# Kernel tuning notes

Hardware: AMD Instinct MI355X
Metric: run time of the kernel (lower is better)

The kernel has to match this reference:

```python
import jax, jax.numpy as jnp
import numpy as np
import math

D_MODEL = 512
D_HEAD = 64
N_HEADS = D_MODEL // D_HEAD  # 8
COND = 768
K = 7        # neighborhood kernel size
EPS = 1e-6


def _rope_freqs():
    # RoPE(dim=d_head//2, n_heads): freqs geometric in [pi, 10*pi), shape [n_heads, d_head//4]
    dim = D_HEAD // 2
    n = N_HEADS * dim // 2
    freqs = jnp.exp(jnp.linspace(math.log(math.pi), math.log(10.0 * math.pi), n + 1)[:-1])
    return freqs.reshape(dim // 2, N_HEADS).T  # [nh, d_head//4]


def _rms_norm(x, scale, eps):
    mean_sq = jnp.mean(x * x, axis=-1, keepdims=True)
    return x * (scale * jax.lax.rsqrt(mean_sq + eps))


def _apply_rotary(x, theta):
    # rotate first 2*d dims of head dim, leave the rest untouched
    d = theta.shape[-1]
    x1, x2, rest = x[..., :d], x[..., d:2 * d], x[..., 2 * d:]
    cos, sin = jnp.cos(theta), jnp.sin(theta)
    return jnp.concatenate([x1 * cos - x2 * sin, x2 * cos + x1 * sin, rest], axis=-1)


def _nb_idx(L, k):
    # NATTEN border handling: window shifts (clamps) so every query sees exactly k keys
    i = np.arange(L)
    start = np.clip(i - k // 2, 0, L - k)
    return jnp.asarray(start[:, None] + np.arange(k)[None, :])  # [L, k]


def setup_inputs() -> dict:
    key = jax.random.key(0)
    ks = jax.random.split(key, 7)
    N, H, W = 2, 32, 32
    x = jax.random.normal(ks[0], (N, H, W, D_MODEL), jnp.float32)
    pos = jax.random.uniform(ks[1], (N, H, W, 1), jnp.float32, -1.0, 1.0)
    cond = jax.random.normal(ks[2], (N, COND), jnp.float32)
    w_cond = jax.random.normal(ks[3], (D_MODEL, COND), jnp.float32) * 0.02
    w_qkv = jax.random.normal(ks[4], (3 * D_MODEL, D_MODEL), jnp.float32) * 0.02
    scale = jnp.full((N_HEADS,), 10.0, jnp.float32)
    w_out = jax.random.normal(ks[5], (D_MODEL, D_MODEL), jnp.float32) * 0.02
    return {"x": x, "pos": pos, "cond": cond, "w_cond": w_cond,
            "w_qkv": w_qkv, "scale": scale, "w_out": w_out}


def reference(x, pos, cond, w_cond, w_qkv, scale, w_out):
    N, H, W, C = x.shape
    skip = x
    # AdaRMSNorm: rms_norm(x, linear(cond) + 1)
    norm_scale = cond @ w_cond.T + 1.0                  # [N, C]
    xn = _rms_norm(x, norm_scale[:, None, None, :], EPS)
    # qkv projection -> [3, N, nh, H, W, e]
    qkv = (xn @ w_qkv.T).reshape(N, H, W, 3, N_HEADS, D_HEAD)
    qkv = qkv.transpose(3, 0, 4, 1, 2, 5)
    q, k, v = qkv[0], qkv[1], qkv[2]                    # [N, nh, H, W, e]
    # cosine-sim scaling
    sq = jnp.sqrt(scale)[:, None, None, None]           # [nh,1,1,1]
    q = q * (sq * jax.lax.rsqrt(jnp.sum(q * q, -1, keepdims=True) + 1e-6))
    k = k * (sq * jax.lax.rsqrt(jnp.sum(k * k, -1, keepdims=True) + 1e-6))
    # RoPE
    theta = pos[..., None, :] * _rope_freqs()           # [N,H,W,nh,e/4]
    theta = jnp.moveaxis(theta, -2, -4)                 # [N,nh,H,W,e/4]
    q = _apply_rotary(q, theta)
    k = _apply_rotary(k, theta)
    # 2D neighborhood attention (NATTEN, dilation 1)
    ih, iw = _nb_idx(H, K), _nb_idx(W, K)
    Knb = k[:, :, ih][:, :, :, :, iw]                   # [N,nh,H,K,W,K,e]
    Vnb = v[:, :, ih][:, :, :, :, iw]
    qk = jnp.einsum('ncije,nciajbe->ncijab', q, Knb)    # [N,nh,H,W,K,K]
    a = jax.nn.softmax(qk.reshape(N, N_HEADS, H, W, K * K), axis=-1)
    a = a.reshape(N, N_HEADS, H, W, K, K)
    o = jnp.einsum('ncijab,nciajbe->ncije', a, Vnb)     # [N,nh,H,W,e]
    o = o.transpose(0, 2, 3, 1, 4).reshape(N, H, W, C)
    return o @ w_out.T + skip
```

## Files before the change

### kernel.cpp

```cpp
#include <hip/hip_runtime.h>

typedef unsigned short u16;
typedef unsigned int u32;
typedef __bf16 bf16x8 __attribute__((ext_vector_type(8)));
typedef float f32x4 __attribute__((ext_vector_type(4)));

__device__ __forceinline__ float bf2f(u16 v) {
    union { u32 u; float f; } c; c.u = ((u32)v) << 16; return c.f;
}
__device__ __forceinline__ u16 f2bf(float f) {
    union { float f; u32 u; } c; c.f = f;
    u32 u = c.u + 0x7fffu + ((c.u >> 16) & 1u);
    return (u16)(u >> 16);
}

__global__ __launch_bounds__(256) void cond_prepw_kernel(
    const float* __restrict__ cond, const float* __restrict__ w_cond, float* __restrict__ ns,
    const float* __restrict__ w_qkv, const float* __restrict__ w_out,
    u16* __restrict__ wqkvb, u16* __restrict__ woutb)
{
    int b = blockIdx.x;
    if (b < 256) {
        int lane = threadIdx.x & 63;
        int wid = b * 4 + (threadIdx.x >> 6);
        int n = wid >> 9, c = wid & 511;
        const float* cp = cond + n * 768;
        const float* wp = w_cond + (size_t)c * 768;
        float s = 0.f;
        #pragma unroll
        for (int j = 0; j < 12; j++)
            s += cp[lane + j * 64] * wp[lane + j * 64];
        #pragma unroll
        for (int d = 1; d < 64; d <<= 1) s += __shfl_xor(s, d);
        if (lane == 0) ns[wid] = s + 1.f;
    } else {
        const float* src; u16* dst; size_t i4;
        if (b < 1024) { src = w_qkv; dst = wqkvb; i4 = (size_t)(b - 256)  * 1024 + threadIdx.x * 4; }
        else          { src = w_out; dst = woutb; i4 = (size_t)(b - 1024) * 1024 + threadIdx.x * 4; }
        float4 v = *(const float4*)(src + i4);
        ushort4 o; o.x = f2bf(v.x); o.y = f2bf(v.y); o.z = f2bf(v.z); o.w = f2bf(v.w);
        *(ushort4*)(dst + i4) = o;
    }
}

__global__ __launch_bounds__(256) void rms_kernel(
    const float* __restrict__ x, const float* __restrict__ ns, u16* __restrict__ xn)
{
    int b = blockIdx.x;
    int w = threadIdx.x >> 6, lane = threadIdx.x & 63;
    int p = b * 4 + w;
    int n = p >> 10;
    const float* xp = x + (size_t)p * 512;
    const float* nsp = ns + n * 512;
    float4 v0 = *(const float4*)(xp + lane * 4);
    float4 v1 = *(const float4*)(xp + 256 + lane * 4);
    float ss = v0.x * v0.x + v0.y * v0.y + v0.z * v0.z + v0.w * v0.w
             + v1.x * v1.x + v1.y * v1.y + v1.z * v1.z + v1.w * v1.w;
    #pragma unroll
    for (int d = 1; d < 64; d <<= 1) ss += __shfl_xor(ss, d);
    float inv = rsqrtf(ss * (1.f / 512.f) + 1e-6f);
    float4 n0 = *(const float4*)(nsp + lane * 4);
    float4 n1 = *(const float4*)(nsp + 256 + lane * 4);
    ushort4 o0, o1;
    o0.x = f2bf(v0.x * n0.x * inv); o0.y = f2bf(v0.y * n0.y * inv);
    o0.z = f2bf(v0.z * n0.z * inv); o0.w = f2bf(v0.w * n0.w * inv);
    o1.x = f2bf(v1.x * n1.x * inv); o1.y = f2bf(v1.y * n1.y * inv);
    o1.z = f2bf(v1.z * n1.z * inv); o1.w = f2bf(v1.w * n1.w * inv);
    *(ushort4*)(xn + (size_t)p * 512 + lane * 4) = o0;
    *(ushort4*)(xn + (size_t)p * 512 + 256 + lane * 4) = o1;
}

__global__ __launch_bounds__(256) void gemm_qkv(
    const u16* __restrict__ A, const u16* __restrict__ B,
    const float* __restrict__ pos, const float* __restrict__ scale,
    u16* __restrict__ qp, u16* __restrict__ kp, u16* __restrict__ vp)
{
    __shared__ __align__(16) u16 As[4][64][40];
    __shared__ __align__(16) u16 Bs[4][64][40];
    int tid = threadIdx.x;
    int lane = tid & 63;
    int w = tid >> 6;
    int wm = w >> 1, wn = w & 1;
    int bm = blockIdx.x * 64, bn = blockIdx.y * 64;
    int qk = blockIdx.y >> 3, h = blockIdx.y & 7;
    int lrow = tid >> 2, lc8 = (tid & 3) * 8;

    f32x4 zero = {0.f, 0.f, 0.f, 0.f};
    f32x4 acc[2][2];
    acc[0][0] = zero; acc[0][1] = zero; acc[1][0] = zero; acc[1][1] = zero;

    const u16* Ap = A + (size_t)(bm + lrow) * 512 + lc8;
    const u16* Bp = B + (size_t)(bn + lrow) * 512 + lc8;
    int m = lane & 15, quad = lane >> 4, kq = quad * 8;

    for (int k0 = 0; k0 < 512; k0 += 128) {
        #pragma unroll
        for (int s = 0; s < 4; s++) {
            *(uint4*)&As[s][lrow][lc8] = *(const uint4*)(Ap + k0 + s * 32);
            *(uint4*)&Bs[s][lrow][lc8] = *(const uint4*)(Bp + k0 + s * 32);
        }
        __syncthreads();
        #pragma unroll
        for (int kk = 0; kk < 4; kk++) {
            bf16x8 a0 = *(const bf16x8*)&As[kk][wm * 32 + m][kq];
            bf16x8 a1 = *(const bf16x8*)&As[kk][wm * 32 + 16 + m][kq];
            bf16x8 b0 = *(const bf16x8*)&Bs[kk][wn * 32 + m][kq];
            bf16x8 b1 = *(const bf16x8*)&Bs[kk][wn * 32 + 16 + m][kq];
            acc[0][0] = __builtin_amdgcn_mfma_f32_16x16x32_bf16(a0, b0, acc[0][0], 0, 0, 0);
            acc[0][1] = __builtin_amdgcn_mfma_f32_16x16x32_bf16(a0, b1, acc[0][1], 0, 0, 0);
            acc[1][0] = __builtin_amdgcn_mfma_f32_16x16x32_bf16(a1, b0, acc[1][0], 0, 0, 0);
            acc[1][1] = __builtin_amdgcn_mfma_f32_16x16x32_bf16(a1, b1, acc[1][1], 0, 0, 0);
        }
        __syncthreads();
    }

    float invn[2][4];
    if (qk < 2) {
        float* red = (float*)As;
        #pragma unroll
        for (int ri = 0; ri < 2; ri++)
        #pragma unroll
        for (int reg = 0; reg < 4; reg++) {
            float pa = acc[ri][0][reg] * acc[ri][0][reg]
                     + acc[ri][1][reg] * acc[ri][1][reg];
            #pragma unroll
            for (int d = 1; d < 16; d <<= 1) pa += __shfl_xor(pa, d);
            if (m == 0) red[(wm * 32 + ri * 16 + quad * 4 + reg) * 2 + wn] = pa;
        }
        __syncthreads();
        float sq = sqrtf(scale[h]);
        #pragma unroll
        for (int ri = 0; ri < 2; ri++)
        #pragma unroll
        for (int reg = 0; reg < 4; reg++) {
            int rl = wm * 32 + ri * 16 + quad * 4 + reg;
            invn[ri][reg] = sq * rsqrtf(red[rl * 2] + red[rl * 2 + 1] + 1e-6f);
        }
    }
    u16* plane = (qk == 0) ? qp : (qk == 1) ? kp : vp;
    float fr = 3.14159265358979323846f * expf((float)(m * 8 + h) * (2.302585092994046f / 128.f));
    #pragma unroll
    for (int ri = 0; ri < 2; ri++)
    #pragma unroll
    for (int reg = 0; reg < 4; reg++) {
        int rl = wm * 32 + ri * 16 + quad * 4 + reg;
        int p = bm + rl;
        size_t basep = ((size_t)((p >> 10) * 8 + h) * 1024 + (p & 1023)) * 64;
        float v0 = acc[ri][0][reg], v1 = acc[ri][1][reg];
        if (qk < 2) {
            float ivn = invn[ri][reg];
            v0 *= ivn; v1 *= ivn;
            if (wn == 0) {
                float th = pos[p] * fr;
                float cs = cosf(th), sn = sinf(th);
                float o0 = v0 * cs - v1 * sn;
                float o1 = v1 * cs + v0 * sn;
                v0 = o0; v1 = o1;
            }
        }
        plane[basep + wn * 32 + m]      = f2bf(v0);
        plane[basep + wn * 32 + 16 + m] = f2bf(v1);
    }
}

__global__ __launch_bounds__(256) void gemm_out(
    const u16* __restrict__ A, const u16* __restrict__ B,
    float* __restrict__ C, const float* __restrict__ skip, int N, int K)
{
    __shared__ __align__(16) u16 As[4][64][40];
    __shared__ __align__(16) u16 Bs[4][64][40];
    int tid = threadIdx.x;
    int lane = tid & 63;
    int w = tid >> 6;
    int wm = w >> 1, wn = w & 1;
    int bm = blockIdx.x * 64, bn = blockIdx.y * 64;
    int lrow = tid >> 2, lc8 = (tid & 3) * 8;

    f32x4 zero = {0.f, 0.f, 0.f, 0.f};
    f32x4 acc[2][2];
    acc[0][0] = zero; acc[0][1] = zero; acc[1][0] = zero; acc[1][1] = zero;

    const u16* Ap = A + (size_t)(bm + lrow) * K + lc8;
    const u16* Bp = B + (size_t)(bn + lrow) * K + lc8;
    int r = lane & 15, kq = (lane >> 4) * 8;

    for (int k0 = 0; k0 < K; k0 += 128) {
        #pragma unroll
        for (int s = 0; s < 4; s++) {
            *(uint4*)&As[s][lrow][lc8] = *(const uint4*)(Ap + k0 + s * 32);
            *(uint4*)&Bs[s][lrow][lc8] = *(const uint4*)(Bp + k0 + s * 32);
        }
        __syncthreads();
        #pragma unroll
        for (int kk = 0; kk < 4; kk++) {
            bf16x8 a0 = *(const bf16x8*)&As[kk][wm * 32 + r][kq];
            bf16x8 a1 = *(const bf16x8*)&As[kk][wm * 32 + 16 + r][kq];
            bf16x8 b0 = *(const bf16x8*)&Bs[kk][wn * 32 + r][kq];
            bf16x8 b1 = *(const bf16x8*)&Bs[kk][wn * 32 + 16 + r][kq];
            acc[0][0] = __builtin_amdgcn_mfma_f32_16x16x32_bf16(a0, b0, acc[0][0], 0, 0, 0);
            acc[0][1] = __builtin_amdgcn_mfma_f32_16x16x32_bf16(a0, b1, acc[0][1], 0, 0, 0);
            acc[1][0] = __builtin_amdgcn_mfma_f32_16x16x32_bf16(a1, b0, acc[1][0], 0, 0, 0);
            acc[1][1] = __builtin_amdgcn_mfma_f32_16x16x32_bf16(a1, b1, acc[1][1], 0, 0, 0);
        }
        __syncthreads();
    }

    #pragma unroll
    for (int ri = 0; ri < 2; ri++)
    #pragma unroll
    for (int ci = 0; ci < 2; ci++) {
        int col = bn + wn * 32 + ci * 16 + (lane & 15);
        int row0 = bm + wm * 32 + ri * 16 + (lane >> 4) * 4;
        #pragma unroll
        for (int reg = 0; reg < 4; reg++) {
            size_t idx = (size_t)(row0 + reg) * N + col;
            C[idx] = acc[ri][ci][reg] + skip[idx];
        }
    }
}

__global__ __launch_bounds__(512) void attn_mfma(
    const u16* __restrict__ qp, const u16* __restrict__ kp, const u16* __restrict__ vp,
    u16* __restrict__ ob)
{
    __shared__ __align__(16) u16 Kb[208 * 72];
    __shared__ __align__(16) u16 Sb[64 * 232];

    int tid = threadIdx.x, lane = tid & 63, w = tid >> 6;
    int bx = blockIdx.x;
    int n = bx >> 7, h = (bx >> 4) & 7, t = bx & 15;
    int ti = (t >> 2) * 8, tj = (t & 3) * 8;
    int r0 = min(max(ti - 3, 0), 18), c0 = min(max(tj - 3, 0), 18);
    const u16* qpl = qp + ((size_t)(n * 8 + h) << 16);
    const u16* kpl = kp + ((size_t)(n * 8 + h) << 16);
    const u16* vpl = vp + ((size_t)(n * 8 + h) << 16);

    for (int g = tid; g < 1568; g += 512) {
        int nb = g >> 3, k8 = (g & 7) << 3;
        int ar = nb / 14, ac = nb - ar * 14;
        *(uint4*)&Kb[nb * 72 + k8] =
            *(const uint4*)&kpl[(size_t)((r0 + ar) * 32 + c0 + ac) * 64 + k8];
    }
    __syncthreads();

    int m = lane & 15, quad = lane >> 4;
    int rg = w & 3, half = w >> 2;
    {
        int r = rg * 16 + m;
        int tok = (ti + (r >> 3)) * 32 + (tj + (r & 7));
        bf16x8 qf0 = *(const bf16x8*)&qpl[(size_t)tok * 64 + quad * 8];
        bf16x8 qf1 = *(const bf16x8*)&qpl[(size_t)tok * 64 + 32 + quad * 8];
        _Float16* sp = (_Float16*)Sb;
        int ntb = half * 7;
        int ntn = 7 - half;
        for (int i = 0; i < ntn; i++) {
            int nt = ntb + i;
            f32x4 acc = {0.f, 0.f, 0.f, 0.f};
            bf16x8 b0 = *(const bf16x8*)&Kb[(nt * 16 + m) * 72 + quad * 8];
            bf16x8 b1 = *(const bf16x8*)&Kb[(nt * 16 + m) * 72 + 32 + quad * 8];
            __builtin_amdgcn_s_setprio(1);
            acc = __builtin_amdgcn_mfma_f32_16x16x32_bf16(qf0, b0, acc, 0, 0, 0);
            acc = __builtin_amdgcn_mfma_f32_16x16x32_bf16(qf1, b1, acc, 0, 0, 0);
            __builtin_amdgcn_s_setprio(0);
            #pragma unroll
            for (int reg = 0; reg < 4; reg++)
                sp[(rg * 16 + quad * 4 + reg) * 232 + nt * 16 + m] = (_Float16)acc[reg];
        }
    }
    __syncthreads();

    for (int g = tid; g < 1568; g += 512) {
        int nb = g >> 3, k8 = (g & 7) << 3;
        int ar = nb / 14, ac = nb - ar * 14;
        uint4 v4 = *(const uint4*)&vpl[(size_t)((r0 + ar) * 32 + c0 + ac) * 64 + k8];
        u32 uu[4] = {v4.x, v4.y, v4.z, v4.w};
        #pragma unroll
        for (int e = 0; e < 4; e++) {
            Kb[(k8 + 2 * e) * 234 + nb]     = (u16)(uu[e] & 0xffff);
            Kb[(k8 + 2 * e + 1) * 234 + nb] = (u16)(uu[e] >> 16);
        }
    }
    for (int g = tid; g < 1792; g += 512) {
        int d = g / 28, nb = 196 + (g - d * 28);
        Kb[d * 234 + nb] = 0;
    }

    {
        int l16 = lane & 15, g4 = lane >> 4;
        #pragma unroll
        for (int it = 0; it < 2; it++) {
            int rr = w * 8 + it * 4 + g4;
            int i2 = ti + (rr >> 3), j2 = tj + (rr & 7);
            int alo = min(max(i2 - 3, 0), 25) - r0;
            int blo = min(max(j2 - 3, 0), 25) - c0;
            const _Float16* sp = (const _Float16*)&Sb[rr * 232];
            float vals[14];
            float mx = -1e30f;
            #pragma unroll
            for (int c = 0; c < 14; c++) {
                int col = l16 + c * 16;
                float v = -1e30f;
                if (col < 196) {
                    int ar = col / 14, ac = col - ar * 14;
                    if (ar >= alo && ar < alo + 7 && ac >= blo && ac < blo + 7)
                        v = (float)sp[col];
                }
                vals[c] = v; mx = fmaxf(mx, v);
            }
            #pragma unroll
            for (int d = 1; d < 16; d <<= 1) mx = fmaxf(mx, __shfl_xor(mx, d));
            float s = 0.f;
            #pragma unroll
            for (int c = 0; c < 14; c++) {
                float e = exp2f((vals[c] - mx) * 1.44269504f);
                vals[c] = e; s += e;
            }
            #pragma unroll
            for (int d = 1; d < 16; d <<= 1) s += __shfl_xor(s, d);
            float rs = __frcp_rn(s);
            u16* pp = &Sb[rr * 232];
            #pragma unroll
            for (int c = 0; c < 14; c++)
                pp[l16 + c * 16] = f2bf(vals[c] * rs);
        }
    }
    __syncthreads();

    f32x4 oacc[2];
    {
        f32x4 z = {0.f, 0.f, 0.f, 0.f};
        oacc[0] = z; oacc[1] = z;
    }
    #pragma unroll
    for (int ks = 0; ks < 7; ks++) {
        bf16x8 pa = *(const bf16x8*)&Sb[(rg * 16 + m) * 232 + ks * 32 + quad * 8];
        __builtin_amdgcn_s_setprio(1);
        #pragma unroll
        for (int j = 0; j < 2; j++) {
            int nt = half * 2 + j;
            int ad = (nt * 16 + m) * 234 + ks * 32 + quad * 8;
            union { u32 u[4]; bf16x8 v; } vb;
            vb.u[0] = *(const u32*)&Kb[ad];
            vb.u[1] = *(const u32*)&Kb[ad + 2];
            vb.u[2] = *(const u32*)&Kb[ad + 4];
            vb.u[3] = *(const u32*)&Kb[ad + 6];
            oacc[j] = __builtin_amdgcn_mfma_f32_16x16x32_bf16(pa, vb.v, oacc[j], 0, 0, 0);
        }
        __builtin_amdgcn_s_setprio(0);
    }
    #pragma unroll
    for (int j = 0; j < 2; j++) {
        int nt = half * 2 + j;
        #pragma unroll
        for (int reg = 0; reg < 4; reg++) {
            int rr = rg * 16 + quad * 4 + reg;
            int tok = (ti + (rr >> 3)) * 32 + (tj + (rr & 7));
            ob[(size_t)(n * 1024 + tok) * 512 + h * 64 + nt * 16 + m] = f2bf(oacc[j][reg]);
        }
    }
}

extern "C" void kernel_launch(void* const* d_in, const int* in_sizes, int n_in,
                              void* d_out, int out_size, void* d_ws, size_t ws_size,
                              hipStream_t stream)
{
    const float *x = nullptr, *pos = nullptr, *cond = nullptr, *w_cond = nullptr,
                *w_qkv = nullptr, *scale = nullptr, *w_out = nullptr;
    for (int i = 0; i < n_in; i++) {
        switch (in_sizes[i]) {
            case 1048576: x      = (const float*)d_in[i]; break;
            case 2048:    pos    = (const float*)d_in[i]; break;
            case 1536:    cond   = (const float*)d_in[i]; break;
            case 393216:  w_cond = (const float*)d_in[i]; break;
            case 786432:  w_qkv  = (const float*)d_in[i]; break;
            case 8:       scale  = (const float*)d_in[i]; break;
            case 262144:  w_out  = (const float*)d_in[i]; break;
            default: break;
        }
    }
    float* out = (float*)d_out;

    char* ws = (char*)d_ws;
    float* ns    = (float*)ws;
    u16*   wqkvb = (u16*)(ws + 12288);
    u16*   woutb = (u16*)(ws + 12288 + 1572864);
    u16*   xn    = (u16*)(ws + 12288 + 2097152);
    u16*   qp    = (u16*)(ws + 12288 + 4194304);
    u16*   kp    = (u16*)(ws + 12288 + 6291456);
    u16*   vp    = (u16*)(ws + 12288 + 8388608);
    u16*   ob    = (u16*)(ws + 12288 + 10485760);

    cond_prepw_kernel<<<1280, 256, 0, stream>>>(cond, w_cond, ns, w_qkv, w_out, wqkvb, woutb);
    rms_kernel<<<512, 256, 0, stream>>>(x, ns, xn);
    gemm_qkv<<<dim3(32, 24), 256, 0, stream>>>(xn, wqkvb, pos, scale, qp, kp, vp);
    attn_mfma<<<256, 512, 0, stream>>>(qp, kp, vp, ob);
    gemm_out<<<dim3(32, 8), 256, 0, stream>>>(ob, woutb, out, x, 512, 512);
}
```

Measured before the change: 105.2 us.

## Fuse all five stages into one cooperative persistent kernel with grid syncs

Replaces the five separate kernel launches (cond/weight prep, RMS norm, QKV GEMM, neighborhood attention, output GEMM) with one cooperative kernel of 256 blocks by 512 threads that runs each stage in turn, separated by grid-wide syncs. The goal is to remove per-launch overhead and the gaps between kernels. In exchange, every stage is fixed to 256 blocks of 512 threads, so some stages run at lower parallelism (the QKV GEMM loops three tiles per block), and each grid sync has its own cost. If the cooperative launch fails, it falls back to the old multi-kernel path.

```diff
diff --git a/kernel.cpp b/kernel.cpp
--- a/kernel.cpp
+++ b/kernel.cpp
@@ -1,4 +1,7 @@
 #include <hip/hip_runtime.h>
+#include <hip/hip_cooperative_groups.h>
+
+namespace cg = cooperative_groups;
 
 typedef unsigned short u16;
 typedef unsigned int u32;
@@ -13,6 +16,328 @@
     u32 u = c.u + 0x7fffu + ((c.u >> 16) & 1u);
     return (u16)(u >> 16);
 }
+
+__global__ __launch_bounds__(512) void fused_all(
+    const float* __restrict__ cond, const float* __restrict__ w_cond,
+    const float* __restrict__ w_qkv, const float* __restrict__ w_out,
+    const float* __restrict__ x, const float* __restrict__ pos,
+    const float* __restrict__ scale,
+    float* __restrict__ ns, u16* __restrict__ wqkvb, u16* __restrict__ woutb,
+    u16* __restrict__ xn, u16* __restrict__ qp, u16* __restrict__ kp,
+    u16* __restrict__ vp, u16* __restrict__ ob, float* __restrict__ out)
+{
+    __shared__ __align__(16) u16 SM[29824];
+    cg::grid_group gg = cg::this_grid();
+
+    int tid = threadIdx.x, lane = tid & 63, w = tid >> 6;
+    int bid = blockIdx.x;
+    int m = lane & 15, quad = lane >> 4, kq = quad * 8;
+
+    if (w < 4) {
+        int wid = bid * 4 + w;
+        int n = wid >> 9, c = wid & 511;
+        const float* cp = cond + n * 768;
+        const float* wp = w_cond + (size_t)c * 768;
+        float s = 0.f;
+        #pragma unroll
+        for (int j = 0; j < 12; j++)
+            s += cp[lane + j * 64] * wp[lane + j * 64];
+        #pragma unroll
+        for (int d = 1; d < 64; d <<= 1) s += __shfl_xor(s, d);
+        if (lane == 0) ns[wid] = s + 1.f;
+    } else {
+        int gt = (bid * 4 + (w - 4)) * 64 + lane;
+        #pragma unroll
+        for (int i = 0; i < 4; i++) {
+            int task = gt + i * 65536;
+            const float* src; u16* dst; int idx;
+            if (task < 196608) { src = w_qkv; dst = wqkvb; idx = task; }
+            else               { src = w_out; dst = woutb; idx = task - 196608; }
+            float4 v = *(const float4*)(src + (size_t)idx * 4);
+            ushort4 o; o.x = f2bf(v.x); o.y = f2bf(v.y); o.z = f2bf(v.z); o.w = f2bf(v.w);
+            *(ushort4*)(dst + (size_t)idx * 4) = o;
+        }
+    }
+    gg.sync();
+
+    {
+        int p = bid * 8 + w;
+        int n = p >> 10;
+        const float* xp = x + (size_t)p * 512;
+        const float* nsp = ns + n * 512;
+        float4 v0 = *(const float4*)(xp + lane * 4);
+        float4 v1 = *(const float4*)(xp + 256 + lane * 4);
+        float ss = v0.x * v0.x + v0.y * v0.y + v0.z * v0.z + v0.w * v0.w
+                 + v1.x * v1.x + v1.y * v1.y + v1.z * v1.z + v1.w * v1.w;
+        #pragma unroll
+        for (int d = 1; d < 64; d <<= 1) ss += __shfl_xor(ss, d);
+        float inv = rsqrtf(ss * (1.f / 512.f) + 1e-6f);
+        float4 n0 = *(const float4*)(nsp + lane * 4);
+        float4 n1 = *(const float4*)(nsp + 256 + lane * 4);
+        ushort4 o0, o1;
+        o0.x = f2bf(v0.x * n0.x * inv); o0.y = f2bf(v0.y * n0.y * inv);
+        o0.z = f2bf(v0.z * n0.z * inv); o0.w = f2bf(v0.w * n0.w * inv);
+        o1.x = f2bf(v1.x * n1.x * inv); o1.y = f2bf(v1.y * n1.y * inv);
+        o1.z = f2bf(v1.z * n1.z * inv); o1.w = f2bf(v1.w * n1.w * inv);
+        *(ushort4*)(xn + (size_t)p * 512 + lane * 4) = o0;
+        *(ushort4*)(xn + (size_t)p * 512 + 256 + lane * 4) = o1;
+    }
+    gg.sync();
+
+    {
+        u16 (*As)[64][40] = (u16 (*)[64][40])SM;
+        u16 (*Bs)[64][40] = (u16 (*)[64][40])(SM + 10240);
+        int wm = w >> 1, wn = w & 1;
+        int lrow = tid >> 3, lc16 = (tid & 7) * 16;
+        int sA = lc16 >> 5, off = lc16 & 31;
+        int rlbase = wm * 16 + quad * 4;
+
+        for (int it = 0; it < 3; it++) {
+            int t = bid + it * 256;
+            int bm = (t & 31) * 64;
+            int by = t >> 5;
+            int bn = by * 64;
+            int qk = by >> 3, h = by & 7;
+            const u16* Ap = xn + (size_t)(bm + lrow) * 512 + lc16;
+            const u16* Bp = wqkvb + (size_t)(bn + lrow) * 512 + lc16;
+            f32x4 acc0 = {0.f, 0.f, 0.f, 0.f};
+            f32x4 acc1 = {0.f, 0.f, 0.f, 0.f};
+            __syncthreads();
+            for (int k0 = 0; k0 < 512; k0 += 128) {
+                *(uint4*)&As[sA][lrow][off]     = *(const uint4*)(Ap + k0);
+                *(uint4*)&As[sA][lrow][off + 8] = *(const uint4*)(Ap + k0 + 8);
+                *(uint4*)&Bs[sA][lrow][off]     = *(const uint4*)(Bp + k0);
+                *(uint4*)&Bs[sA][lrow][off + 8] = *(const uint4*)(Bp + k0 + 8);
+                __syncthreads();
+                #pragma unroll
+                for (int kk = 0; kk < 4; kk++) {
+                    bf16x8 a  = *(const bf16x8*)&As[kk][wm * 16 + m][kq];
+                    bf16x8 b0 = *(const bf16x8*)&Bs[kk][wn * 32 + m][kq];
+                    bf16x8 b1 = *(const bf16x8*)&Bs[kk][wn * 32 + 16 + m][kq];
+                    acc0 = __builtin_amdgcn_mfma_f32_16x16x32_bf16(a, b0, acc0, 0, 0, 0);
+                    acc1 = __builtin_amdgcn_mfma_f32_16x16x32_bf16(a, b1, acc1, 0, 0, 0);
+                }
+                __syncthreads();
+            }
+            float invn[4];
+            if (qk < 2) {
+                float* red = (float*)SM;
+                #pragma unroll
+                for (int reg = 0; reg < 4; reg++) {
+                    float pa = acc0[reg] * acc0[reg] + acc1[reg] * acc1[reg];
+                    #pragma unroll
+                    for (int d = 1; d < 16; d <<= 1) pa += __shfl_xor(pa, d);
+                    if (m == 0) red[(rlbase + reg) * 2 + wn] = pa;
+                }
+                __syncthreads();
+                float sq = sqrtf(scale[h]);
+                #pragma unroll
+                for (int reg = 0; reg < 4; reg++) {
+                    int rl = rlbase + reg;
+                    invn[reg] = sq * rsqrtf(red[rl * 2] + red[rl * 2 + 1] + 1e-6f);
+                }
+            }
+            u16* plane = (qk == 0) ? qp : (qk == 1) ? kp : vp;
+            float fr = 3.14159265358979323846f * expf((float)(m * 8 + h) * (2.302585092994046f / 128.f));
+            #pragma unroll
+            for (int reg = 0; reg < 4; reg++) {
+                int rl = rlbase + reg;
+                int p = bm + rl;
+                size_t basep = ((size_t)((p >> 10) * 8 + h) * 1024 + (p & 1023)) * 64;
+                float v0 = acc0[reg], v1 = acc1[reg];
+                if (qk < 2) {
+                    float ivn = invn[reg];
+                    v0 *= ivn; v1 *= ivn;
+                    if (wn == 0) {
+                        float th = pos[p] * fr;
+                        float cs = cosf(th), sn = sinf(th);
+                        float o0 = v0 * cs - v1 * sn;
+                        float o1 = v1 * cs + v0 * sn;
+                        v0 = o0; v1 = o1;
+                    }
+                }
+                plane[basep + wn * 32 + m]      = f2bf(v0);
+                plane[basep + wn * 32 + 16 + m] = f2bf(v1);
+            }
+        }
+    }
+    gg.sync();
+
+    {
+        u16* Kb = SM;
+        u16* Sb = SM + 14976;
+        int n = bid >> 7, h = (bid >> 4) & 7, t = bid & 15;
+        int ti = (t >> 2) * 8, tj = (t & 3) * 8;
+        int r0 = min(max(ti - 3, 0), 18), c0 = min(max(tj - 3, 0), 18);
+        const u16* qpl = qp + ((size_t)(n * 8 + h) << 16);
+        const u16* kpl = kp + ((size_t)(n * 8 + h) << 16);
+        const u16* vpl = vp + ((size_t)(n * 8 + h) << 16);
+
+        __syncthreads();
+        for (int g = tid; g < 1568; g += 512) {
+            int nb = g >> 3, k8 = (g & 7) << 3;
+            int ar = nb / 14, ac = nb - ar * 14;
+            *(uint4*)&Kb[nb * 72 + k8] =
+                *(const uint4*)&kpl[(size_t)((r0 + ar) * 32 + c0 + ac) * 64 + k8];
+        }
+        __syncthreads();
+
+        int rg = w & 3, half = w >> 2;
+        {
+            int r = rg * 16 + m;
+            int tok = (ti + (r >> 3)) * 32 + (tj + (r & 7));
+            bf16x8 qf0 = *(const bf16x8*)&qpl[(size_t)tok * 64 + quad * 8];
+            bf16x8 qf1 = *(const bf16x8*)&qpl[(size_t)tok * 64 + 32 + quad * 8];
+            _Float16* sp = (_Float16*)Sb;
+            int ntb = half * 7;
+            int ntn = 7 - half;
+            for (int i = 0; i < ntn; i++) {
+                int nt = ntb + i;
+                f32x4 acc = {0.f, 0.f, 0.f, 0.f};
+                bf16x8 b0 = *(const bf16x8*)&Kb[(nt * 16 + m) * 72 + quad * 8];
+                bf16x8 b1 = *(const bf16x8*)&Kb[(nt * 16 + m) * 72 + 32 + quad * 8];
+                __builtin_amdgcn_s_setprio(1);
+                acc = __builtin_amdgcn_mfma_f32_16x16x32_bf16(qf0, b0, acc, 0, 0, 0);
+                acc = __builtin_amdgcn_mfma_f32_16x16x32_bf16(qf1, b1, acc, 0, 0, 0);
+                __builtin_amdgcn_s_setprio(0);
+                #pragma unroll
+                for (int reg = 0; reg < 4; reg++)
+                    sp[(rg * 16 + quad * 4 + reg) * 232 + nt * 16 + m] = (_Float16)acc[reg];
+            }
+        }
+        __syncthreads();
+
+        for (int g = tid; g < 1568; g += 512) {
+            int nb = g >> 3, k8 = (g & 7) << 3;
+            int ar = nb / 14, ac = nb - ar * 14;
+            uint4 v4 = *(const uint4*)&vpl[(size_t)((r0 + ar) * 32 + c0 + ac) * 64 + k8];
+            u32 uu[4] = {v4.x, v4.y, v4.z, v4.w};
+            #pragma unroll
+            for (int e = 0; e < 4; e++) {
+                Kb[(k8 + 2 * e) * 234 + nb]     = (u16)(uu[e] & 0xffff);
+                Kb[(k8 + 2 * e + 1) * 234 + nb] = (u16)(uu[e] >> 16);
+            }
+        }
+        for (int g = tid; g < 1792; g += 512) {
+            int d = g / 28, nb = 196 + (g - d * 28);
+            Kb[d * 234 + nb] = 0;
+        }
+
+        {
+            int l16 = lane & 15, g4 = lane >> 4;
+            #pragma unroll
+            for (int it = 0; it < 2; it++) {
+                int rr = w * 8 + it * 4 + g4;
+                int i2 = ti + (rr >> 3), j2 = tj + (rr & 7);
+                int alo = min(max(i2 - 3, 0), 25) - r0;
+                int blo = min(max(j2 - 3, 0), 25) - c0;
+                const _Float16* sp = (const _Float16*)&Sb[rr * 232];
+                float vals[14];
+                float mx = -1e30f;
+                #pragma unroll
+                for (int c = 0; c < 14; c++) {
+                    int col = l16 + c * 16;
+                    float v = -1e30f;
+                    if (col < 196) {
+                        int ar = col / 14, ac = col - ar * 14;
+                        if (ar >= alo && ar < alo + 7 && ac >= blo && ac < blo + 7)
+                            v = (float)sp[col];
+                    }
+                    vals[c] = v; mx = fmaxf(mx, v);
+                }
+                #pragma unroll
+                for (int d = 1; d < 16; d <<= 1) mx = fmaxf(mx, __shfl_xor(mx, d));
+                float s = 0.f;
+                #pragma unroll
+                for (int c = 0; c < 14; c++) {
+                    float e = exp2f((vals[c] - mx) * 1.44269504f);
+                    vals[c] = e; s += e;
+                }
+                #pragma unroll
+                for (int d = 1; d < 16; d <<= 1) s += __shfl_xor(s, d);
+                float rs = __frcp_rn(s);
+                u16* pp = &Sb[rr * 232];
+                #pragma unroll
+                for (int c = 0; c < 14; c++)
+                    pp[l16 + c * 16] = f2bf(vals[c] * rs);
+            }
+        }
+        __syncthreads();
+
+        f32x4 oacc[2];
+        {
+            f32x4 z = {0.f, 0.f, 0.f, 0.f};
+            oacc[0] = z; oacc[1] = z;
+        }
+        #pragma unroll
+        for (int ks = 0; ks < 7; ks++) {
+            bf16x8 pa = *(const bf16x8*)&Sb[(rg * 16 + m) * 232 + ks * 32 + quad * 8];
+            __builtin_amdgcn_s_setprio(1);
+            #pragma unroll
+            for (int j = 0; j < 2; j++) {
+                int nt = half * 2 + j;
+                int ad = (nt * 16 + m) * 234 + ks * 32 + quad * 8;
+                union { u32 u[4]; bf16x8 v; } vb;
+                vb.u[0] = *(const u32*)&Kb[ad];
+                vb.u[1] = *(const u32*)&Kb[ad + 2];
+                vb.u[2] = *(const u32*)&Kb[ad + 4];
+                vb.u[3] = *(const u32*)&Kb[ad + 6];
+                oacc[j] = __builtin_amdgcn_mfma_f32_16x16x32_bf16(pa, vb.v, oacc[j], 0, 0, 0);
+            }
+            __builtin_amdgcn_s_setprio(0);
+        }
+        #pragma unroll
+        for (int j = 0; j < 2; j++) {
+            int nt = half * 2 + j;
+            #pragma unroll
+            for (int reg = 0; reg < 4; reg++) {
+                int rr = rg * 16 + quad * 4 + reg;
+                int tok = (ti + (rr >> 3)) * 32 + (tj + (rr & 7));
+                ob[(size_t)(n * 1024 + tok) * 512 + h * 64 + nt * 16 + m] = f2bf(oacc[j][reg]);
+            }
+        }
+    }
+    gg.sync();
+
+    {
+        u16 (*As)[64][40] = (u16 (*)[64][40])SM;
+        u16 (*Bs)[64][40] = (u16 (*)[64][40])(SM + 10240);
+        int wm = w >> 1, wn = w & 1;
+        int lrow = tid >> 3, lc16 = (tid & 7) * 16;
+        int sA = lc16 >> 5, off = lc16 & 31;
+        int bm = (bid & 31) * 64, bn = (bid >> 5) * 64;
+        const u16* Ap = ob + (size_t)(bm + lrow) * 512 + lc16;
+        const u16* Bp = woutb + (size_t)(bn + lrow) * 512 + lc16;
+        f32x4 acc0 = {0.f, 0.f, 0.f, 0.f};
+        f32x4 acc1 = {0.f, 0.f, 0.f, 0.f};
+        __syncthreads();
+        for (int k0 = 0; k0 < 512; k0 += 128) {
+            *(uint4*)&As[sA][lrow][off]     = *(const uint4*)(Ap + k0);
+            *(uint4*)&As[sA][lrow][off + 8] = *(const uint4*)(Ap + k0 + 8);
+            *(uint4*)&Bs[sA][lrow][off]     = *(const uint4*)(Bp + k0);
+            *(uint4*)&Bs[sA][lrow][off + 8] = *(const uint4*)(Bp + k0 + 8);
+            __syncthreads();
+            #pragma unroll
+            for (int kk = 0; kk < 4; kk++) {
+                bf16x8 a  = *(const bf16x8*)&As[kk][wm * 16 + m][kq];
+                bf16x8 b0 = *(const bf16x8*)&Bs[kk][wn * 32 + m][kq];
+                bf16x8 b1 = *(const bf16x8*)&Bs[kk][wn * 32 + 16 + m][kq];
+                acc0 = __builtin_amdgcn_mfma_f32_16x16x32_bf16(a, b0, acc0, 0, 0, 0);
+                acc1 = __builtin_amdgcn_mfma_f32_16x16x32_bf16(a, b1, acc1, 0, 0, 0);
+            }
+            __syncthreads();
+        }
+        #pragma unroll
+        for (int reg = 0; reg < 4; reg++) {
+            int row = bm + wm * 16 + quad * 4 + reg;
+            int col = bn + wn * 32 + m;
+            size_t i0 = (size_t)row * 512 + col;
+            out[i0]      = acc0[reg] + x[i0];
+            out[i0 + 16] = acc1[reg] + x[i0 + 16];
+        }
+    }
+}
+
 
 __global__ __launch_bounds__(256) void cond_prepw_kernel(
     const float* __restrict__ cond, const float* __restrict__ w_cond, float* __restrict__ ns,
@@ -390,9 +715,20 @@
     u16*   vp    = (u16*)(ws + 12288 + 8388608);
     u16*   ob    = (u16*)(ws + 12288 + 10485760);
 
-    cond_prepw_kernel<<<1280, 256, 0, stream>>>(cond, w_cond, ns, w_qkv, w_out, wqkvb, woutb);
-    rms_kernel<<<512, 256, 0, stream>>>(x, ns, xn);
-    gemm_qkv<<<dim3(32, 24), 256, 0, stream>>>(xn, wqkvb, pos, scale, qp, kp, vp);
-    attn_mfma<<<256, 512, 0, stream>>>(qp, kp, vp, ob);
-    gemm_out<<<dim3(32, 8), 256, 0, stream>>>(ob, woutb, out, x, 512, 512);
-}
+    void* args[] = {
+        (void*)&cond, (void*)&w_cond, (void*)&w_qkv, (void*)&w_out,
+        (void*)&x, (void*)&pos, (void*)&scale,
+        (void*)&ns, (void*)&wqkvb, (void*)&woutb, (void*)&xn,
+        (void*)&qp, (void*)&kp, (void*)&vp, (void*)&ob, (void*)&out
+    };
+    hipError_t e = hipLaunchCooperativeKernel((const void*)fused_all,
+                                              dim3(256), dim3(512),
+                                              args, 0, stream);
+    if (e != hipSuccess) {
+        cond_prepw_kernel<<<1280, 256, 0, stream>>>(cond, w_cond, ns, w_qkv, w_out, wqkvb, woutb);
+        rms_kernel<<<512, 256, 0, stream>>>(x, ns, xn);
+        gemm_qkv<<<dim3(32, 24), 256, 0, stream>>>(xn, wqkvb, pos, scale, qp, kp, vp);
+        attn_mfma<<<256, 512, 0, stream>>>(qp, kp, vp, ob);
+        gemm_out<<<dim3(32, 8), 256, 0, stream>>>(ob, woutb, out, x, 512, 512);
+    }
+}
```

New measurement: 244.1 us. 2.32x slower.

## Fold AdaRMSNorm scale into per-batch QKV weights and merge prep kernels

Applied to the files above, without the earlier changes.

The per-channel conditioning scale is folded into a per-batch copy of the bf16 QKV weight, so the RMS-norm pass only applies the row rsqrt. This removes the dependency between the cond linear and the norm, which lets cond, weight conversion and RMS normalisation run in one launch instead of two. The QKV GEMM picks the weight copy for its batch from the block row. In exchange the weight buffer doubles and each cond dot product is recomputed by the blocks that share a channel slice.

```diff
diff --git a/kernel.cpp b/kernel.cpp
--- a/kernel.cpp
+++ b/kernel.cpp
@@ -14,60 +14,71 @@
     return (u16)(u >> 16);
 }
 
-__global__ __launch_bounds__(256) void cond_prepw_kernel(
-    const float* __restrict__ cond, const float* __restrict__ w_cond, float* __restrict__ ns,
+__global__ __launch_bounds__(256) void prep_kernel(
+    const float* __restrict__ cond, const float* __restrict__ w_cond,
     const float* __restrict__ w_qkv, const float* __restrict__ w_out,
-    u16* __restrict__ wqkvb, u16* __restrict__ woutb)
+    const float* __restrict__ x,
+    u16* __restrict__ wqkvb2, u16* __restrict__ woutb, u16* __restrict__ xn)
 {
     int b = blockIdx.x;
-    if (b < 256) {
-        int lane = threadIdx.x & 63;
-        int wid = b * 4 + (threadIdx.x >> 6);
-        int n = wid >> 9, c = wid & 511;
-        const float* cp = cond + n * 768;
-        const float* wp = w_cond + (size_t)c * 768;
+    int t = threadIdx.x;
+    if (b < 192) {
+        __shared__ float ns_s[32];
+        int n  = b / 96;
+        int rc = (b / 16) % 6;
+        int p16 = b & 15;
+        int c0 = p16 * 32;
+        int cl = t >> 3, g = t & 7;
+        const float* cp = cond + n * 768 + g * 96;
+        const float* wp = w_cond + (size_t)(c0 + cl) * 768 + g * 96;
         float s = 0.f;
         #pragma unroll
-        for (int j = 0; j < 12; j++)
-            s += cp[lane + j * 64] * wp[lane + j * 64];
-        #pragma unroll
-        for (int d = 1; d < 64; d <<= 1) s += __shfl_xor(s, d);
-        if (lane == 0) ns[wid] = s + 1.f;
+        for (int j = 0; j < 24; j++) {
+            float4 a = *(const float4*)(cp + j * 4);
+            float4 w4 = *(const float4*)(wp + j * 4);
+            s += a.x * w4.x + a.y * w4.y + a.z * w4.z + a.w * w4.w;
+        }
+        s += __shfl_xor(s, 1); s += __shfl_xor(s, 2); s += __shfl_xor(s, 4);
+        if (g == 0) ns_s[cl] = s + 1.f;
+        __syncthreads();
+        #pragma unroll
+        for (int i = 0; i < 8; i++) {
+            int task = i * 256 + t;
+            int row = rc * 256 + (task >> 3);
+            int cg = task & 7;
+            const float* src = w_qkv + (size_t)row * 512 + c0 + cg * 4;
+            float4 v = *(const float4*)src;
+            float s0 = ns_s[cg * 4], s1 = ns_s[cg * 4 + 1],
+                  s2 = ns_s[cg * 4 + 2], s3 = ns_s[cg * 4 + 3];
+            ushort4 o;
+            o.x = f2bf(v.x * s0); o.y = f2bf(v.y * s1);
+            o.z = f2bf(v.z * s2); o.w = f2bf(v.w * s3);
+            *(ushort4*)(wqkvb2 + (size_t)n * 786432 + (size_t)row * 512 + c0 + cg * 4) = o;
+        }
+    } else if (b < 448) {
+        size_t i4 = (size_t)(b - 192) * 1024 + t * 4;
+        float4 v = *(const float4*)(w_out + i4);
+        ushort4 o; o.x = f2bf(v.x); o.y = f2bf(v.y); o.z = f2bf(v.z); o.w = f2bf(v.w);
+        *(ushort4*)(woutb + i4) = o;
     } else {
-        const float* src; u16* dst; size_t i4;
-        if (b < 1024) { src = w_qkv; dst = wqkvb; i4 = (size_t)(b - 256)  * 1024 + threadIdx.x * 4; }
-        else          { src = w_out; dst = woutb; i4 = (size_t)(b - 1024) * 1024 + threadIdx.x * 4; }
-        float4 v = *(const float4*)(src + i4);
-        ushort4 o; o.x = f2bf(v.x); o.y = f2bf(v.y); o.z = f2bf(v.z); o.w = f2bf(v.w);
-        *(ushort4*)(dst + i4) = o;
-    }
-}
-
-__global__ __launch_bounds__(256) void rms_kernel(
-    const float* __restrict__ x, const float* __restrict__ ns, u16* __restrict__ xn)
-{
-    int b = blockIdx.x;
-    int w = threadIdx.x >> 6, lane = threadIdx.x & 63;
-    int p = b * 4 + w;
-    int n = p >> 10;
-    const float* xp = x + (size_t)p * 512;
-    const float* nsp = ns + n * 512;
-    float4 v0 = *(const float4*)(xp + lane * 4);
-    float4 v1 = *(const float4*)(xp + 256 + lane * 4);
-    float ss = v0.x * v0.x + v0.y * v0.y + v0.z * v0.z + v0.w * v0.w
-             + v1.x * v1.x + v1.y * v1.y + v1.z * v1.z + v1.w * v1.w;
-    #pragma unroll
-    for (int d = 1; d < 64; d <<= 1) ss += __shfl_xor(ss, d);
-    float inv = rsqrtf(ss * (1.f / 512.f) + 1e-6f);
-    float4 n0 = *(const float4*)(nsp + lane * 4);
-    float4 n1 = *(const float4*)(nsp + 256 + lane * 4);
-    ushort4 o0, o1;
-    o0.x = f2bf(v0.x * n0.x * inv); o0.y = f2bf(v0.y * n0.y * inv);
-    o0.z = f2bf(v0.z * n0.z * inv); o0.w = f2bf(v0.w * n0.w * inv);
-    o1.x = f2bf(v1.x * n1.x * inv); o1.y = f2bf(v1.y * n1.y * inv);
-    o1.z = f2bf(v1.z * n1.z * inv); o1.w = f2bf(v1.w * n1.w * inv);
-    *(ushort4*)(xn + (size_t)p * 512 + lane * 4) = o0;
-    *(ushort4*)(xn + (size_t)p * 512 + 256 + lane * 4) = o1;
+        int w = t >> 6, lane = t & 63;
+        int p = (b - 448) * 4 + w;
+        const float* xp = x + (size_t)p * 512;
+        float4 v0 = *(const float4*)(xp + lane * 4);
+        float4 v1 = *(const float4*)(xp + 256 + lane * 4);
+        float ss = v0.x * v0.x + v0.y * v0.y + v0.z * v0.z + v0.w * v0.w
+                 + v1.x * v1.x + v1.y * v1.y + v1.z * v1.z + v1.w * v1.w;
+        #pragma unroll
+        for (int d = 1; d < 64; d <<= 1) ss += __shfl_xor(ss, d);
+        float inv = rsqrtf(ss * (1.f / 512.f) + 1e-6f);
+        ushort4 o0, o1;
+        o0.x = f2bf(v0.x * inv); o0.y = f2bf(v0.y * inv);
+        o0.z = f2bf(v0.z * inv); o0.w = f2bf(v0.w * inv);
+        o1.x = f2bf(v1.x * inv); o1.y = f2bf(v1.y * inv);
+        o1.z = f2bf(v1.z * inv); o1.w = f2bf(v1.w * inv);
+        *(ushort4*)(xn + (size_t)p * 512 + lane * 4) = o0;
+        *(ushort4*)(xn + (size_t)p * 512 + 256 + lane * 4) = o1;
+    }
 }
 
 __global__ __launch_bounds__(256) void gemm_qkv(
@@ -90,7 +101,7 @@
     acc[0][0] = zero; acc[0][1] = zero; acc[1][0] = zero; acc[1][1] = zero;
 
     const u16* Ap = A + (size_t)(bm + lrow) * 512 + lc8;
-    const u16* Bp = B + (size_t)(bn + lrow) * 512 + lc8;
+    const u16* Bp = B + (size_t)(blockIdx.x >> 4) * 786432 + (size_t)(bn + lrow) * 512 + lc8;
     int m = lane & 15, quad = lane >> 4, kq = quad * 8;
 
     for (int k0 = 0; k0 < 512; k0 += 128) {
@@ -381,18 +392,16 @@
     float* out = (float*)d_out;
 
     char* ws = (char*)d_ws;
-    float* ns    = (float*)ws;
-    u16*   wqkvb = (u16*)(ws + 12288);
-    u16*   woutb = (u16*)(ws + 12288 + 1572864);
-    u16*   xn    = (u16*)(ws + 12288 + 2097152);
-    u16*   qp    = (u16*)(ws + 12288 + 4194304);
-    u16*   kp    = (u16*)(ws + 12288 + 6291456);
-    u16*   vp    = (u16*)(ws + 12288 + 8388608);
-    u16*   ob    = (u16*)(ws + 12288 + 10485760);
-
-    cond_prepw_kernel<<<1280, 256, 0, stream>>>(cond, w_cond, ns, w_qkv, w_out, wqkvb, woutb);
-    rms_kernel<<<512, 256, 0, stream>>>(x, ns, xn);
-    gemm_qkv<<<dim3(32, 24), 256, 0, stream>>>(xn, wqkvb, pos, scale, qp, kp, vp);
+    u16* wqkvb2 = (u16*)ws;
+    u16* woutb  = (u16*)(ws + 3145728);
+    u16* xn     = (u16*)(ws + 3670016);
+    u16* qp     = (u16*)(ws + 5767168);
+    u16* kp     = (u16*)(ws + 7864320);
+    u16* vp     = (u16*)(ws + 9961472);
+    u16* ob     = (u16*)(ws + 12058624);
+
+    prep_kernel<<<960, 256, 0, stream>>>(cond, w_cond, w_qkv, w_out, x, wqkvb2, woutb, xn);
+    gemm_qkv<<<dim3(32, 24), 256, 0, stream>>>(xn, wqkvb2, pos, scale, qp, kp, vp);
     attn_mfma<<<256, 512, 0, stream>>>(qp, kp, vp, ob);
     gemm_out<<<dim3(32, 8), 256, 0, stream>>>(ob, woutb, out, x, 512, 512);
 }
```

New measurement: 108.6 us. 3.2% more time.
